# Optimization experiments

Measured on AMD Instinct MI355X. Metric: run time of the kernel, lower is better.

The kernel has to match this reference:

```python
import jax, jax.numpy as jnp
import numpy as np

N_HEADS, N_KV, HEAD_DIM = 16, 4, 64
DIM = 4096
LATENT = N_HEADS * HEAD_DIM   # 1024
KV_DIM = N_KV * HEAD_DIM      # 256
KSZ = 3


def _causal_conv1d(x, w, b, groups):
    # x: [B,S,C]; w: [Cout, Cin//groups, K]; causal left padding (K-1)
    y = jax.lax.conv_general_dilated(
        x.transpose(0, 2, 1), w, window_strides=(1,),
        padding=[(w.shape[-1] - 1, 0)], feature_group_count=groups,
        dimension_numbers=('NCH', 'OIH', 'NCH'))
    return (y + b[None, :, None]).transpose(0, 2, 1)


def _rope(x, cos, sin):
    # x: [B,H,S,D] interleaved pairs; cos/sin: [1,1,S,D//2]
    x1, x2 = x[..., ::2], x[..., 1::2]
    out = jnp.stack([x1 * cos - x2 * sin, x1 * sin + x2 * cos], axis=-1)
    return out.reshape(x.shape)


def _l2norm(x):
    n = jnp.sqrt(jnp.sum(x * x, axis=-1, keepdims=True))
    return x / jnp.maximum(n, 1e-12)


def setup_inputs() -> dict:
    key = jax.random.key(0)
    ks = jax.random.split(key, 12)
    sc = 0.02
    x = jax.random.normal(ks[0], (2, 2048, DIM), jnp.float32)
    w_qkv = jax.random.normal(ks[1], (LATENT + 2 * KV_DIM, DIM), jnp.float32) * sc
    w_o = jax.random.normal(ks[2], (DIM, LATENT), jnp.float32) * sc
    qc1_w = jax.random.normal(ks[3], (LATENT, LATENT // N_HEADS, KSZ), jnp.float32) * sc
    qc1_b = jnp.zeros((LATENT,), jnp.float32)
    qc2_w = jax.random.normal(ks[4], (LATENT, LATENT, KSZ), jnp.float32) * sc
    qc2_b = jnp.zeros((LATENT,), jnp.float32)
    kc1_w = jax.random.normal(ks[5], (KV_DIM, KV_DIM // N_KV, KSZ), jnp.float32) * sc
    kc1_b = jnp.zeros((KV_DIM,), jnp.float32)
    kc2_w = jax.random.normal(ks[6], (KV_DIM, KV_DIM, KSZ), jnp.float32) * sc
    kc2_b = jnp.zeros((KV_DIM,), jnp.float32)
    key_temp = jnp.full((1,), float(HEAD_DIM) ** 0.5, jnp.float32)
    return dict(x=x, w_qkv=w_qkv, w_o=w_o, qc1_w=qc1_w, qc1_b=qc1_b,
                qc2_w=qc2_w, qc2_b=qc2_b, kc1_w=kc1_w, kc1_b=kc1_b,
                kc2_w=kc2_w, kc2_b=kc2_b, key_temp=key_temp)


def _forward(x, w_qkv, w_o, qc1_w, qc1_b, qc2_w, qc2_b, kc1_w, kc1_b, kc2_w, kc2_b, key_temp):
    B, S, _ = x.shape
    qkv = x @ w_qkv.T  # [B,S,LATENT+2*KV_DIM]
    q = qkv[..., :LATENT]
    k = qkv[..., LATENT:LATENT + KV_DIM]
    # value shift: first half current token, second half previous token (0 at t=0)
    half = KV_DIM // 2
    v_curr = qkv[..., LATENT + KV_DIM:LATENT + KV_DIM + half]
    v_prev = qkv[..., LATENT + KV_DIM + half:]
    v = jnp.concatenate([v_curr, jnp.pad(v_prev[:, :-1, :], ((0, 0), (1, 0), (0, 0)))], axis=-1)
    q_pre, k_pre = q, k
    # grouped causal conv sequences on q and k
    q = _causal_conv1d(_causal_conv1d(q, qc1_w, qc1_b, N_HEADS), qc2_w, qc2_b, 1)
    k = _causal_conv1d(_causal_conv1d(k, kc1_w, kc1_b, N_KV), kc2_w, kc2_b, 1)
    # qk-mean coupling (n_groups = 4 branch)
    q_mean = q_pre.reshape(B, S, N_HEADS, HEAD_DIM).mean(axis=2)  # [B,S,hd]
    k_mean = k_pre.reshape(B, S, N_KV, HEAD_DIM).mean(axis=2)
    q = q.reshape(B, S, N_HEADS, HEAD_DIM) + 0.5 * k_mean[:, :, None, :]
    k = k.reshape(B, S, N_KV, HEAD_DIM) + 0.5 * q_mean[:, :, None, :]
    q = q.transpose(0, 2, 1, 3)                                   # [B,H,S,d]
    k = k.transpose(0, 2, 1, 3)                                   # [B,Hkv,S,d]
    v = v.reshape(B, S, N_KV, HEAD_DIM).transpose(0, 2, 1, 3)
    # qk-norm with learned key temperature
    q = _l2norm(q)
    k = _l2norm(k) * key_temp
    # RoPE (interleaved pairs)
    inv = 1.0 / (10000.0 ** (jnp.arange(0, HEAD_DIM, 2, dtype=jnp.float32) / HEAD_DIM))
    ang = jnp.arange(S, dtype=jnp.float32)[:, None] * inv[None, :]  # [S,d/2]
    cos, sin = jnp.cos(ang)[None, None], jnp.sin(ang)[None, None]
    q = _rope(q, cos, sin)
    k = _rope(k, cos, sin)
    # GQA: each kv head repeated n_groups times contiguously
    kg = jnp.repeat(k, N_HEADS // N_KV, axis=1)
    vg = jnp.repeat(v, N_HEADS // N_KV, axis=1)
    scale = HEAD_DIM ** -0.5
    scores = jnp.einsum('bhqd,bhkd->bhqk', q, kg) * scale
    causal = jnp.tril(jnp.ones((S, S), dtype=bool))
    scores = jnp.where(causal[None, None], scores, jnp.finfo(scores.dtype).min)
    attn = jax.nn.softmax(scores, axis=-1)
    out = jnp.einsum('bhqk,bhkd->bhqd', attn, vg)
    out = out.transpose(0, 2, 1, 3).reshape(B, S, LATENT)
    return out @ w_o.T  # output_scale = 1.0


def reference(x, w_qkv, w_o, qc1_w, qc1_b, qc2_w, qc2_b, kc1_w, kc1_b, kc2_w, kc2_b, key_temp):
    return _forward(x, w_qkv, w_o, qc1_w, qc1_b, qc2_w, qc2_b, kc1_w, kc1_b, kc2_w, kc2_b, key_temp)
```

## Files before the change

kernel.cpp:

```cpp
#include <hip/hip_runtime.h>
#include <hip/hip_bf16.h>
#include <cstddef>

#define NB 2
#define SEQ 2048
#define DIMX 4096
#define NH 16
#define NKV 4
#define HD 64
#define LATENT 1024
#define KVD 256
#define QKVN 1536
#define BS (NB*SEQ)
#define SP (SEQ+2)

typedef __attribute__((ext_vector_type(8))) short short8v;
typedef __attribute__((ext_vector_type(4))) float f32x4;
typedef __attribute__((ext_vector_type(4))) unsigned short ushort4v;
typedef __attribute__((ext_vector_type(4))) unsigned int uint4v;

static __device__ __forceinline__ unsigned short f2bf(float f) {
    union { float f; unsigned u; } v; v.f = f;
    unsigned r = v.u + 0x7fffu + ((v.u >> 16) & 1u);
    return (unsigned short)(r >> 16);
}

static __device__ __forceinline__ unsigned cvt_pk_bf16(float lo, float hi) {
    unsigned r;
    asm("v_cvt_pk_bf16_f32 %0, %1, %2" : "=v"(r) : "v"(lo), "v"(hi));
    return r;
}

static __device__ __forceinline__ void gload_lds16(const unsigned short* g, unsigned short* l) {
    __builtin_amdgcn_global_load_lds((const __attribute__((address_space(1))) void*)g,
                                     (__attribute__((address_space(3))) void*)l, 16, 0, 0);
}

#define XC_BLK (BS*DIMX/4/256)
#define WC_BLK (QKVN*DIMX/4/256)
__global__ __launch_bounds__(256)
void cast_inputs(const float* __restrict__ x, unsigned short* __restrict__ xb,
                 const float* __restrict__ wq, unsigned short* __restrict__ wqb)
{
    const int blk = blockIdx.x;
    const float* in; unsigned short* out; int i;
    if (blk < XC_BLK) { in = x; out = xb; i = blk * 256 + threadIdx.x; }
    else              { in = wq; out = wqb; i = (blk - XC_BLK) * 256 + threadIdx.x; }
    const float4 v = *reinterpret_cast<const float4*>(in + (size_t)i * 4);
    ushort4v o = {f2bf(v.x), f2bf(v.y), f2bf(v.z), f2bf(v.w)};
    *reinterpret_cast<ushort4v*>(out + (size_t)i * 4) = o;
}

#define WO_BLK 4096
#define QW_N (LATENT*LATENT*3)
#define QW_BLK 12288
#define KW_N (KVD*KVD*3)
#define KW_BLK 768
#define RT_BLK 256
__global__ __launch_bounds__(256)
void prep_misc(const float* __restrict__ wo, unsigned short* __restrict__ wob,
               const float* __restrict__ qc2w, unsigned short* __restrict__ qc2wr,
               const float* __restrict__ kc2w, unsigned short* __restrict__ kc2wr,
               float2* __restrict__ rtab,
               unsigned short* __restrict__ pq, unsigned short* __restrict__ pk)
{
    const int blk = blockIdx.x, tid = threadIdx.x;
    if (blk < WO_BLK) {
        const int i = blk * 256 + tid;
        const float4 v = *reinterpret_cast<const float4*>(wo + (size_t)i * 4);
        ushort4v o = {f2bf(v.x), f2bf(v.y), f2bf(v.z), f2bf(v.w)};
        *reinterpret_cast<ushort4v*>(wob + (size_t)i * 4) = o;
    } else if (blk < WO_BLK + QW_BLK) {
        const int idx = (blk - WO_BLK) * 256 + tid;
        if (idx < QW_N) {
            const int o = idx / (LATENT * 3), rem = idx % (LATENT * 3);
            const int j = rem / LATENT, c = rem % LATENT;
            qc2wr[idx] = f2bf(qc2w[(size_t)o * LATENT * 3 + c * 3 + j]);
        }
    } else if (blk < WO_BLK + QW_BLK + KW_BLK) {
        const int idx = (blk - WO_BLK - QW_BLK) * 256 + tid;
        if (idx < KW_N) {
            const int o = idx / (KVD * 3), rem = idx % (KVD * 3);
            const int j = rem / KVD, c = rem % KVD;
            kc2wr[idx] = f2bf(kc2w[(size_t)o * KVD * 3 + c * 3 + j]);
        }
    } else if (blk < WO_BLK + QW_BLK + KW_BLK + RT_BLK) {
        const int idx = (blk - WO_BLK - QW_BLK - KW_BLK) * 256 + tid;
        const int s = idx >> 5, i = idx & 31;
        const float inv = powf(10000.f, -(float)(2 * i) * (1.f / HD));
        const float ang = (float)s * inv;
        rtab[idx] = make_float2(cosf(ang), sinf(ang));
    } else {
        const int t = (blk - WO_BLK - QW_BLK - KW_BLK - RT_BLK) * 256 + tid;
        if (t < 2 * 2 * LATENT) {
            const int b = t / (2 * LATENT), r = (t % (2 * LATENT)) / LATENT, c = t % LATENT;
            pq[((size_t)b * SP + r) * LATENT + c] = 0;
        }
        if (t < 2 * 2 * KVD) {
            const int b = t / (2 * KVD), r = (t % (2 * KVD)) / KVD, c = t % KVD;
            pk[((size_t)b * SP + r) * KVD + c] = 0;
        }
    }
}

template<int CONV>
__global__ __launch_bounds__(256)
void gemm_bf16(const unsigned short* __restrict__ A, const unsigned short* __restrict__ W,
               const float* __restrict__ bias, float* __restrict__ C,
               int M, int N, int K, int Cch, int klen, size_t ps1, size_t ps2)
{
    __shared__ unsigned short Abuf[2][128 * 32];
    __shared__ unsigned short Bbuf[2][128 * 32];
    const int gx = gridDim.x;
    const int nwg = gx * gridDim.y;
    const int lin = blockIdx.y * gx + blockIdx.x;
    const int swz = (lin & 7) * (nwg >> 3) + (lin >> 3);
    const int n0 = (swz % gx) * 128, m0 = (swz / gx) * 128;
    const int koff = blockIdx.z * klen;
    C += (blockIdx.z == 1) ? ps1 : (blockIdx.z == 2 ? ps2 : 0);
    const int tid = threadIdx.x;
    const int wave = tid >> 6, lane = tid & 63;
    const int lg = lane >> 4, lr = lane & 15;
    const int wm = (wave & 1) * 64, wn = (wave >> 1) * 64;
    const int sr = wave * 32 + (lane >> 2);
    const int sc = (lane & 3) * 8;
    const int bb = m0 / SEQ, s0 = m0 % SEQ;

    const int NT = klen / 32;
    f32x4 acc[4][4];
    #pragma unroll
    for (int i = 0; i < 4; i++)
        #pragma unroll
        for (int j = 0; j < 4; j++) acc[i][j] = (f32x4){0.f, 0.f, 0.f, 0.f};

    auto stage = [&](int buf, int kt) {
        const int k0 = koff + kt * 32;
        const unsigned short* ga0;
        if (!CONV) {
            ga0 = A + (size_t)(m0 + sr) * K + k0 + sc;
        } else {
            const int j = k0 / Cch, c0 = k0 - j * Cch;
            ga0 = A + (size_t)(bb * SP + s0 + j + sr) * Cch + c0 + sc;
        }
        const unsigned short* gb0 = W + (size_t)(n0 + sr) * K + k0 + sc;
        const size_t astep = (size_t)16 * (CONV ? Cch : K);
        #pragma unroll
        for (int i = 0; i < 2; i++) {
            gload_lds16(ga0 + i * astep, &Abuf[buf][(wave * 2 + i) * 512]);
            gload_lds16(gb0 + (size_t)i * 16 * K, &Bbuf[buf][(wave * 2 + i) * 512]);
        }
    };

    stage(0, 0);
    __syncthreads();
    int cur = 0;
    for (int kt = 0; kt < NT; ++kt) {
        if (kt + 1 < NT) stage(cur ^ 1, kt + 1);
        short8v af[4], bf[4];
        #pragma unroll
        for (int mi = 0; mi < 4; mi++)
            af[mi] = *reinterpret_cast<const short8v*>(&Abuf[cur][(wm + mi * 16 + lr) * 32 + lg * 8]);
        #pragma unroll
        for (int ni = 0; ni < 4; ni++)
            bf[ni] = *reinterpret_cast<const short8v*>(&Bbuf[cur][(wn + ni * 16 + lr) * 32 + lg * 8]);
        #pragma unroll
        for (int mi = 0; mi < 4; mi++)
            #pragma unroll
            for (int ni = 0; ni < 4; ni++)
                acc[mi][ni] = __builtin_amdgcn_mfma_f32_16x16x32_bf16(af[mi], bf[ni], acc[mi][ni], 0, 0, 0);
        __syncthreads();
        cur ^= 1;
    }

    #pragma unroll
    for (int ni = 0; ni < 4; ni++) {
        const int col = n0 + wn + ni * 16 + lr;
        const float bv = bias ? bias[col] : 0.f;
        #pragma unroll
        for (int mi = 0; mi < 4; mi++)
            #pragma unroll
            for (int r = 0; r < 4; r++)
                C[(size_t)(m0 + wm + mi * 16 + lg * 4 + r) * N + col] = acc[mi][ni][r] + bv;
    }
}

__global__ __launch_bounds__(256)
void conv1_grouped(const float* __restrict__ qkv0, const float* __restrict__ qkv1,
                   const float* __restrict__ qw, const float* __restrict__ qb,
                   const float* __restrict__ kw, const float* __restrict__ kb,
                   unsigned short* __restrict__ pq, unsigned short* __restrict__ pk)
{
    const int t0 = blockIdx.x * 64;
    const int b  = blockIdx.y;
    const int z  = blockIdx.z;
    const bool isq = (z < NH);
    const int g  = isq ? z : z - NH;
    const int coloff = isq ? 0 : LATENT;
    const float* w = isq ? qw : kw;
    const float* bias = isq ? qb : kb;
    unsigned short* out = isq ? pq : pk;
    const int CH = isq ? LATENT : KVD;

    __shared__ float xs[66][64];
    for (int idx = threadIdx.x; idx < 66 * 64; idx += 256) {
        const int i = idx >> 6, ic = idx & 63;
        const int tt = t0 + i - 2;
        float v = 0.f;
        if (tt >= 0) {
            const size_t off = (size_t)(b * SEQ + tt) * QKVN + coloff + g * 64 + ic;
            v = qkv0[off] + qkv1[off];
        }
        xs[i][ic] = v;
    }
    __syncthreads();
    const int oc = threadIdx.x & 63;
    const int ibase = (threadIdx.x >> 6) * 16;
    float acc[16];
    const float bv = bias[g * 64 + oc];
    #pragma unroll
    for (int i = 0; i < 16; i++) acc[i] = bv;
    const float* wp = w + (size_t)(g * 64 + oc) * 192;
    for (int ic = 0; ic < 64; ic++) {
        const float w0 = wp[ic * 3 + 0], w1 = wp[ic * 3 + 1], w2 = wp[ic * 3 + 2];
        float xv[18];
        #pragma unroll
        for (int r = 0; r < 18; r++) xv[r] = xs[ibase + r][ic];
        #pragma unroll
        for (int i = 0; i < 16; i++) acc[i] += w0 * xv[i] + w1 * xv[i + 1] + w2 * xv[i + 2];
    }
    #pragma unroll
    for (int i = 0; i < 16; i++)
        out[((size_t)b * SP + 2 + t0 + ibase + i) * CH + g * 64 + oc] = f2bf(acc[i]);
}

__global__ __launch_bounds__(256)
void meanv_vtrans(const float* __restrict__ qkv0, const float* __restrict__ qkv1,
                  float* __restrict__ qmean, float* __restrict__ kmean,
                  unsigned short* __restrict__ vTb)
{
    const int s0 = blockIdx.x * 16;
    const int b  = blockIdx.y;
    const int tid = threadIdx.x;
    const int w = tid >> 6, d = tid & 63;
    __shared__ unsigned short vt[4][16][72];

    #pragma unroll
    for (int i = 0; i < 4; i++) {
        const int s = s0 + w * 4 + i;
        const int t = b * SEQ + s;
        const float* r0 = qkv0 + (size_t)t * QKVN;
        const float* r1 = qkv1 + (size_t)t * QKVN;
        float qs = 0.f;
        #pragma unroll
        for (int h = 0; h < NH; h++) qs += r0[h * 64 + d] + r1[h * 64 + d];
        qmean[(size_t)t * 64 + d] = qs * (1.f / NH);
        float ks = 0.f;
        #pragma unroll
        for (int h = 0; h < NKV; h++) ks += r0[LATENT + h * 64 + d] + r1[LATENT + h * 64 + d];
        kmean[(size_t)t * 64 + d] = ks * (1.f / NKV);
        #pragma unroll
        for (int g = 0; g < 4; g++) {
            float v;
            if (g < 2) {
                v = r0[LATENT + KVD + g * 64 + d] + r1[LATENT + KVD + g * 64 + d];
            } else {
                v = 0.f;
                if (s > 0) {
                    const size_t off = (size_t)(t - 1) * QKVN + LATENT + KVD + 128 + (g - 2) * 64 + d;
                    v = qkv0[off] + qkv1[off];
                }
            }
            vt[g][w * 4 + i][d] = f2bf(v);
        }
    }
    __syncthreads();
    {
        const int g = tid >> 6, dd = tid & 63;
        short8v o0, o1;
        #pragma unroll
        for (int j = 0; j < 8; j++) { o0[j] = (short)vt[g][j][dd]; o1[j] = (short)vt[g][8 + j][dd]; }
        unsigned short* op = vTb + ((size_t)(b * NKV + g) * 64 + dd) * SEQ + s0;
        *reinterpret_cast<short8v*>(op) = o0;
        *reinterpret_cast<short8v*>(op + 8) = o1;
    }
}

__global__ __launch_bounds__(256)
void qk_final(const float* __restrict__ qc2a, const float* __restrict__ qc2b, const float* __restrict__ qc2c,
              const float* __restrict__ kc2a, const float* __restrict__ kc2b,
              const float* __restrict__ qbias, const float* __restrict__ kbias,
              const float* __restrict__ qmean, const float* __restrict__ kmean,
              const float* __restrict__ key_temp, const float2* __restrict__ rtab,
              unsigned short* __restrict__ qTb, unsigned short* __restrict__ kTb)
{
    const int t = blockIdx.x * 4 + (threadIdx.x >> 6);
    const int hh = blockIdx.y;
    const int d = threadIdx.x & 63;
    const int b = t >> 11, s = t & (SEQ - 1);
    float val;
    if (hh < NH) {
        const size_t off = (size_t)t * LATENT + hh * 64 + d;
        val = qc2a[off] + qc2b[off] + qc2c[off] + qbias[hh * 64 + d] + 0.5f * kmean[t * 64 + d];
    } else {
        const size_t off = (size_t)t * KVD + (hh - NH) * 64 + d;
        val = kc2a[off] + kc2b[off] + kbias[(hh - NH) * 64 + d] + 0.5f * qmean[t * 64 + d];
    }
    float ss = val * val;
    #pragma unroll
    for (int off = 32; off >= 1; off >>= 1) ss += __shfl_xor(ss, off);
    const float n = sqrtf(ss);
    val = val / fmaxf(n, 1e-12f);
    if (hh >= NH) val *= key_temp[0];
    const float2 cs = rtab[s * 32 + (d >> 1)];
    const float cv = cs.x, sv = cs.y;
    const float partner = __shfl_xor(val, 1);
    const float x1 = (d & 1) ? partner : val;
    const float x2 = (d & 1) ? val : partner;
    const float o = (d & 1) ? (x1 * sv + x2 * cv) : (x1 * cv - x2 * sv);
    if (hh < NH) qTb[((size_t)(b * NH + hh) * SEQ + s) * 64 + d] = f2bf(o);
    else         kTb[((size_t)(b * NKV + (hh - NH)) * SEQ + s) * 64 + d] = f2bf(o);
}

__global__ __launch_bounds__(256)
void attn_mfma(const unsigned short* __restrict__ qTb, const unsigned short* __restrict__ kTb,
               const unsigned short* __restrict__ vTb,
               unsigned short* __restrict__ pnum, float* __restrict__ pden)
{
    const int wg = blockIdx.x;
    const int qg = wg >> 8;
    const int u = wg & 255;
    const int xcd = u & 7, i = u >> 3;
    const int bh = (xcd << 2) | (i >> 3);
    const int r = i & 7;
    const int p = (qg == 0) ? r : (qg == 1) ? (15 - r) : (qg == 2) ? (16 + r) : (31 - r);
    const int blk = 15 - (p >> 1);
    const int part = p & 1;
    const int half = blk + 1;
    const int cbeg = part * half, cend = cbeg + half;

    const int b = bh >> 4, h = bh & 15, g = h >> 2;
    const int tid = threadIdx.x;
    const int wave = tid >> 6, lane = tid & 63;
    const int lg = lane >> 4, lr = lane & 15;
    const int qt = blk * 4 + wave;
    const int q0 = qt * 32;

    __shared__ __align__(16) unsigned short SB[2][16][512];

    short8v qf[2][2];
    const unsigned short* qbase = qTb + ((size_t)(b * NH + h) * SEQ + q0) * 64;
    #pragma unroll
    for (int mf = 0; mf < 2; mf++)
        #pragma unroll
        for (int dc = 0; dc < 2; dc++)
            qf[mf][dc] = *reinterpret_cast<const short8v*>(qbase + (size_t)(mf * 16 + lr) * 64 + dc * 32 + lg * 8);

    short8v onesf;
    #pragma unroll
    for (int j = 0; j < 8; j++) onesf[j] = (short)0x3F80;

    f32x4 acc[2][4];
    f32x4 accden[2];
    #pragma unroll
    for (int mf = 0; mf < 2; mf++) {
        accden[mf] = (f32x4){0.f, 0.f, 0.f, 0.f};
        #pragma unroll
        for (int dt = 0; dt < 4; dt++) acc[mf][dt] = (f32x4){0.f, 0.f, 0.f, 0.f};
    }

    const unsigned short* kbase = kTb + (size_t)(b * NKV + g) * SEQ * 64;
    const unsigned short* vbase = vTb + (size_t)(b * NKV + g) * 64 * SEQ;
    const float EC = 0.125f * 1.44269504f;
    const int src01 = ((lg & 1) << 5) + lr;
    const int src23 = src01 + 16;
    const bool hi = (lg >= 2);

    auto stage64 = [&](int buf, int cc) {
        const int kb = cc * 64;
        #pragma unroll
        for (int i2 = 0; i2 < 4; i2++) {
            const int ch = wave * 4 + i2;
            const int st = ch >> 3, chl = ch & 7;
            const int k0 = kb + st * 32;
            const unsigned short* src;
            if (chl < 4) src = kbase + (size_t)(k0 + (chl >> 1) * 16 + lr) * 64 + (chl & 1) * 32 + lg * 8;
            else         src = vbase + (size_t)((chl - 4) * 16 + lr) * SEQ + k0 + lg * 8;
            gload_lds16(src, &SB[buf][ch][lane * 8]);
        }
    };

    stage64(0, cbeg);
    __syncthreads();
    int cur = 0;
    for (int cc = cbeg; cc < cend; ++cc) {
        if (cc + 1 < cend) stage64(cur ^ 1, cc + 1);
        #pragma unroll
        for (int st = 0; st < 2; ++st) {
            const int c = cc * 2 + st;
            if (c > qt) continue;
            const int k0 = c * 32;
            short8v kf[2][2], vf[4];
            #pragma unroll
            for (int kt = 0; kt < 2; kt++)
                #pragma unroll
                for (int dc = 0; dc < 2; dc++)
                    kf[kt][dc] = *reinterpret_cast<const short8v*>(&SB[cur][st * 8 + kt * 2 + dc][lane * 8]);
            #pragma unroll
            for (int dt = 0; dt < 4; dt++)
                vf[dt] = *reinterpret_cast<const short8v*>(&SB[cur][st * 8 + 4 + dt][lane * 8]);

            const bool diag = (c == qt);
            #pragma unroll
            for (int mf = 0; mf < 2; mf++) {
                f32x4 z0 = (f32x4){0.f, 0.f, 0.f, 0.f}, z1 = (f32x4){0.f, 0.f, 0.f, 0.f};
                __builtin_amdgcn_s_setprio(1);
                z0 = __builtin_amdgcn_mfma_f32_16x16x32_bf16(kf[0][0], qf[mf][0], z0, 0, 0, 0);
                z0 = __builtin_amdgcn_mfma_f32_16x16x32_bf16(kf[0][1], qf[mf][1], z0, 0, 0, 0);
                z1 = __builtin_amdgcn_mfma_f32_16x16x32_bf16(kf[1][0], qf[mf][0], z1, 0, 0, 0);
                z1 = __builtin_amdgcn_mfma_f32_16x16x32_bf16(kf[1][1], qf[mf][1], z1, 0, 0, 0);
                __builtin_amdgcn_s_setprio(0);
                float p0[4], p1[4];
                #pragma unroll
                for (int rr = 0; rr < 4; rr++) {
                    p0[rr] = exp2f(z0[rr] * EC);
                    p1[rr] = exp2f(z1[rr] * EC);
                }
                if (diag) {
                    const int q = q0 + mf * 16 + lr;
                    #pragma unroll
                    for (int rr = 0; rr < 4; rr++) {
                        if (k0 + 4 * lg + rr > q)      p0[rr] = 0.f;
                        if (k0 + 16 + 4 * lg + rr > q) p1[rr] = 0.f;
                    }
                }
                const unsigned W00 = cvt_pk_bf16(p0[0], p0[1]);
                const unsigned W01 = cvt_pk_bf16(p0[2], p0[3]);
                const unsigned W10 = cvt_pk_bf16(p1[0], p1[1]);
                const unsigned W11 = cvt_pk_bf16(p1[2], p1[3]);
                const unsigned a0 = __shfl(W00, src01), b0 = __shfl(W10, src01);
                const unsigned a1 = __shfl(W01, src01), b1 = __shfl(W11, src01);
                const unsigned a2 = __shfl(W00, src23), b2 = __shfl(W10, src23);
                const unsigned a3 = __shfl(W01, src23), b3 = __shfl(W11, src23);
                uint4v pw;
                pw.x = hi ? b0 : a0;
                pw.y = hi ? b1 : a1;
                pw.z = hi ? b2 : a2;
                pw.w = hi ? b3 : a3;
                const short8v pa = __builtin_bit_cast(short8v, pw);
                __builtin_amdgcn_s_setprio(1);
                #pragma unroll
                for (int dt = 0; dt < 4; dt++)
                    acc[mf][dt] = __builtin_amdgcn_mfma_f32_16x16x32_bf16(pa, vf[dt], acc[mf][dt], 0, 0, 0);
                accden[mf] = __builtin_amdgcn_mfma_f32_16x16x32_bf16(pa, onesf, accden[mf], 0, 0, 0);
                __builtin_amdgcn_s_setprio(0);
            }
        }
        __syncthreads();
        cur ^= 1;
    }

    const int base = ((bh * 64 + qt) * 2 + part);
    if (lr == 0) {
        #pragma unroll
        for (int mf = 0; mf < 2; mf++)
            #pragma unroll
            for (int rr = 0; rr < 4; rr++)
                pden[base * 32 + mf * 16 + 4 * lg + rr] = accden[mf][rr];
    }
    unsigned short* np = pnum + (size_t)base * 2048;
    #pragma unroll
    for (int mf = 0; mf < 2; mf++)
        #pragma unroll
        for (int dt = 0; dt < 4; dt++)
            #pragma unroll
            for (int rr = 0; rr < 4; rr++)
                np[(mf * 16 + 4 * lg + rr) * 64 + dt * 16 + lr] = f2bf(acc[mf][dt][rr]);
}

__global__ __launch_bounds__(256)
void attn_merge(const unsigned short* __restrict__ pnum, const float* __restrict__ pden,
                unsigned short* __restrict__ attnb)
{
    const int idx = blockIdx.x * 256 + threadIdx.x;
    const int d0 = (idx & 7) * 8;
    const int qr = (idx >> 3) & 31;
    const int qt = (idx >> 8) & 63;
    const int bh = idx >> 14;
    const int base = (bh * 64 + qt) * 2;
    const float den = pden[base * 32 + qr] + pden[(base + 1) * 32 + qr];
    const float inv = 1.f / den;
    const short8v n0 = *reinterpret_cast<const short8v*>(pnum + (size_t)base * 2048 + qr * 64 + d0);
    const short8v n1 = *reinterpret_cast<const short8v*>(pnum + (size_t)(base + 1) * 2048 + qr * 64 + d0);
    short8v ov;
    #pragma unroll
    for (int j = 0; j < 8; j++) {
        union { unsigned u; float f; } t0, t1;
        t0.u = ((unsigned)(unsigned short)n0[j]) << 16;
        t1.u = ((unsigned)(unsigned short)n1[j]) << 16;
        ov[j] = (short)f2bf((t0.f + t1.f) * inv);
    }
    const int q = qt * 32 + qr;
    const int b = bh >> 4, h = bh & 15;
    *reinterpret_cast<short8v*>(attnb + (size_t)(b * SEQ + q) * LATENT + h * 64 + d0) = ov;
}

extern "C" void kernel_launch(void* const* d_in, const int* in_sizes, int n_in,
                              void* d_out, int out_size, void* d_ws, size_t ws_size,
                              hipStream_t stream)
{
    const float* x       = (const float*)d_in[0];
    const float* w_qkv   = (const float*)d_in[1];
    const float* w_o     = (const float*)d_in[2];
    const float* qc1_w   = (const float*)d_in[3];
    const float* qc1_b   = (const float*)d_in[4];
    const float* qc2_w   = (const float*)d_in[5];
    const float* qc2_b   = (const float*)d_in[6];
    const float* kc1_w   = (const float*)d_in[7];
    const float* kc1_b   = (const float*)d_in[8];
    const float* kc2_w   = (const float*)d_in[9];
    const float* kc2_b   = (const float*)d_in[10];
    const float* key_temp = (const float*)d_in[11];

    char* wsb = (char*)d_ws;
    float* qkv = (float*)wsb;                 wsb += (size_t)BS * QKVN * 4;
    float* qc2 = qkv;
    float* kc2 = (float*)((char*)qkv + (size_t)BS * LATENT * 4);
    unsigned short* pq  = (unsigned short*)wsb;  wsb += (size_t)NB * SP * LATENT * 2;
    unsigned short* pk  = (unsigned short*)wsb;  wsb += (size_t)NB * SP * KVD * 2;
    float* qmean = (float*)wsb;  wsb += (size_t)BS * HD * 4;
    float* kmean = (float*)wsb;  wsb += (size_t)BS * HD * 4;
    unsigned short* qTb  = (unsigned short*)wsb;  wsb += (size_t)BS * LATENT * 2;
    unsigned short* kTb  = (unsigned short*)wsb;  wsb += (size_t)BS * KVD * 2;
    unsigned short* vRow = (unsigned short*)wsb;  wsb += (size_t)BS * KVD * 2;
    unsigned short* vTb  = (unsigned short*)wsb;  wsb += (size_t)BS * KVD * 2;
    unsigned short* xb   = (unsigned short*)wsb;  wsb += (size_t)BS * DIMX * 2;
    unsigned short* attnb  = xb;
    unsigned short* qc2wr  = (unsigned short*)((char*)xb + (size_t)BS * LATENT * 2);
    unsigned short* kc2wr  = (unsigned short*)((char*)qc2wr + (size_t)LATENT * LATENT * 3 * 2);
    unsigned short* wqkvb = (unsigned short*)wsb;  wsb += (size_t)QKVN * DIMX * 2;
    unsigned short* wob   = wqkvb;
    (void)vRow;

    float* outp = (float*)d_out;

    float* qkvp1 = outp;
    const size_t QKV_PS = (size_t)((ptrdiff_t)(qkvp1 - qkv));
    float* qc2p1 = (float*)((char*)d_ws + 67512320);
    float* qc2p2 = outp;
    const size_t QC2_PS1 = (size_t)(qc2p1 - qc2);
    const size_t QC2_PS2 = (size_t)((ptrdiff_t)(qc2p2 - qc2));
    float* kc2p1 = (float*)((char*)d_ws + (size_t)BS * QKVN * 4);
    const size_t KC2_PS1 = (size_t)(kc2p1 - kc2);
    float2* rtab = (float2*)((char*)d_ws + 84289536);
    unsigned short* apnum = (unsigned short*)d_ws;
    float* apden = (float*)((char*)d_ws + 16777216);

    cast_inputs<<<dim3(XC_BLK + WC_BLK), 256, 0, stream>>>(x, xb, w_qkv, wqkvb);
    gemm_bf16<0><<<dim3(QKVN / 128, BS / 128, 2), 256, 0, stream>>>(xb, wqkvb, nullptr, qkv, BS, QKVN, DIMX, 0, DIMX / 2, QKV_PS, 0);
    prep_misc<<<dim3(WO_BLK + QW_BLK + KW_BLK + RT_BLK + 16), 256, 0, stream>>>(
        w_o, wob, qc2_w, qc2wr, kc2_w, kc2wr, rtab, pq, pk);
    meanv_vtrans<<<dim3(SEQ / 16, NB), 256, 0, stream>>>(qkv, qkvp1, qmean, kmean, vTb);
    conv1_grouped<<<dim3(SEQ / 64, NB, NH + NKV), 256, 0, stream>>>(qkv, qkvp1, qc1_w, qc1_b, kc1_w, kc1_b, pq, pk);
    gemm_bf16<1><<<dim3(LATENT / 128, BS / 128, 3), 256, 0, stream>>>(pq, qc2wr, nullptr, qc2, BS, LATENT, LATENT * 3, LATENT, LATENT, QC2_PS1, QC2_PS2);
    gemm_bf16<1><<<dim3(KVD / 128, BS / 128, 2), 256, 0, stream>>>(pk, kc2wr, nullptr, kc2, BS, KVD, KVD * 3, KVD, KVD * 3 / 2, KC2_PS1, 0);
    qk_final<<<dim3(BS / 4, NH + NKV), 256, 0, stream>>>(qc2, qc2p1, qc2p2, kc2, kc2p1, qc2_b, kc2_b,
                                                         qmean, kmean, key_temp, rtab, qTb, kTb);
    attn_mfma<<<dim3(1024), 256, 0, stream>>>(qTb, kTb, vTb, apnum, apden);
    attn_merge<<<dim3(2048), 256, 0, stream>>>(apnum, apden, attnb);
    gemm_bf16<0><<<dim3(DIMX / 128, BS / 128, 1), 256, 0, stream>>>(attnb, wob, nullptr, outp, BS, DIMX, LATENT, 0, LATENT, 0, 0);
}
```

Before: 339.0 us.

## Split attention KV range into four parts per query block

The attention kernel now splits each query block's causal KV range into four partitions instead of two and launches twice as many workgroups, ordering them longest-first. The merge kernel sums four partial numerators and denominators. The intent is better load balance and occupancy across CUs on the attention stage. The cost is extra partial-result traffic, a heavier merge, and some empty partitions for short rows.

```diff
diff --git a/kernel.cpp b/kernel.cpp
--- a/kernel.cpp
+++ b/kernel.cpp
@@ -327,16 +327,16 @@
                unsigned short* __restrict__ pnum, float* __restrict__ pden)
 {
     const int wg = blockIdx.x;
-    const int qg = wg >> 8;
+    const int o = wg >> 8;
     const int u = wg & 255;
     const int xcd = u & 7, i = u >> 3;
     const int bh = (xcd << 2) | (i >> 3);
-    const int r = i & 7;
-    const int p = (qg == 0) ? r : (qg == 1) ? (15 - r) : (qg == 2) ? (16 + r) : (31 - r);
-    const int blk = 15 - (p >> 1);
-    const int part = p & 1;
-    const int half = blk + 1;
-    const int cbeg = part * half, cend = cbeg + half;
+    const int rr0 = i & 7;
+    const int v = (o < 4) ? (63 - ((o << 3) + rr0)) : (((o - 4) << 3) + rr0);
+    const int blk = v >> 2;
+    const int part = v & 3;
+    const int T = 2 * (blk + 1);
+    const int cbeg = (part * T) >> 2, cend = ((part + 1) * T) >> 2;
 
     const int b = bh >> 4, h = bh & 15, g = h >> 2;
     const int tid = threadIdx.x;
@@ -389,77 +389,79 @@
         }
     };
 
-    stage64(0, cbeg);
-    __syncthreads();
-    int cur = 0;
-    for (int cc = cbeg; cc < cend; ++cc) {
-        if (cc + 1 < cend) stage64(cur ^ 1, cc + 1);
-        #pragma unroll
-        for (int st = 0; st < 2; ++st) {
-            const int c = cc * 2 + st;
-            if (c > qt) continue;
-            const int k0 = c * 32;
-            short8v kf[2][2], vf[4];
+    if (cbeg < cend) {
+        stage64(0, cbeg);
+        __syncthreads();
+        int cur = 0;
+        for (int cc = cbeg; cc < cend; ++cc) {
+            if (cc + 1 < cend) stage64(cur ^ 1, cc + 1);
             #pragma unroll
-            for (int kt = 0; kt < 2; kt++)
+            for (int st = 0; st < 2; ++st) {
+                const int c = cc * 2 + st;
+                if (c > qt) continue;
+                const int k0 = c * 32;
+                short8v kf[2][2], vf[4];
                 #pragma unroll
-                for (int dc = 0; dc < 2; dc++)
-                    kf[kt][dc] = *reinterpret_cast<const short8v*>(&SB[cur][st * 8 + kt * 2 + dc][lane * 8]);
-            #pragma unroll
-            for (int dt = 0; dt < 4; dt++)
-                vf[dt] = *reinterpret_cast<const short8v*>(&SB[cur][st * 8 + 4 + dt][lane * 8]);
-
-            const bool diag = (c == qt);
-            #pragma unroll
-            for (int mf = 0; mf < 2; mf++) {
-                f32x4 z0 = (f32x4){0.f, 0.f, 0.f, 0.f}, z1 = (f32x4){0.f, 0.f, 0.f, 0.f};
-                __builtin_amdgcn_s_setprio(1);
-                z0 = __builtin_amdgcn_mfma_f32_16x16x32_bf16(kf[0][0], qf[mf][0], z0, 0, 0, 0);
-                z0 = __builtin_amdgcn_mfma_f32_16x16x32_bf16(kf[0][1], qf[mf][1], z0, 0, 0, 0);
-                z1 = __builtin_amdgcn_mfma_f32_16x16x32_bf16(kf[1][0], qf[mf][0], z1, 0, 0, 0);
-                z1 = __builtin_amdgcn_mfma_f32_16x16x32_bf16(kf[1][1], qf[mf][1], z1, 0, 0, 0);
-                __builtin_amdgcn_s_setprio(0);
-                float p0[4], p1[4];
+                for (int kt = 0; kt < 2; kt++)
+                    #pragma unroll
+                    for (int dc = 0; dc < 2; dc++)
+                        kf[kt][dc] = *reinterpret_cast<const short8v*>(&SB[cur][st * 8 + kt * 2 + dc][lane * 8]);
                 #pragma unroll
-                for (int rr = 0; rr < 4; rr++) {
-                    p0[rr] = exp2f(z0[rr] * EC);
-                    p1[rr] = exp2f(z1[rr] * EC);
-                }
-                if (diag) {
-                    const int q = q0 + mf * 16 + lr;
+                for (int dt = 0; dt < 4; dt++)
+                    vf[dt] = *reinterpret_cast<const short8v*>(&SB[cur][st * 8 + 4 + dt][lane * 8]);
+
+                const bool diag = (c == qt);
+                #pragma unroll
+                for (int mf = 0; mf < 2; mf++) {
+                    f32x4 z0 = (f32x4){0.f, 0.f, 0.f, 0.f}, z1 = (f32x4){0.f, 0.f, 0.f, 0.f};
+                    __builtin_amdgcn_s_setprio(1);
+                    z0 = __builtin_amdgcn_mfma_f32_16x16x32_bf16(kf[0][0], qf[mf][0], z0, 0, 0, 0);
+                    z0 = __builtin_amdgcn_mfma_f32_16x16x32_bf16(kf[0][1], qf[mf][1], z0, 0, 0, 0);
+                    z1 = __builtin_amdgcn_mfma_f32_16x16x32_bf16(kf[1][0], qf[mf][0], z1, 0, 0, 0);
+                    z1 = __builtin_amdgcn_mfma_f32_16x16x32_bf16(kf[1][1], qf[mf][1], z1, 0, 0, 0);
+                    __builtin_amdgcn_s_setprio(0);
+                    float p0[4], p1[4];
                     #pragma unroll
                     for (int rr = 0; rr < 4; rr++) {
-                        if (k0 + 4 * lg + rr > q)      p0[rr] = 0.f;
-                        if (k0 + 16 + 4 * lg + rr > q) p1[rr] = 0.f;
+                        p0[rr] = exp2f(z0[rr] * EC);
+                        p1[rr] = exp2f(z1[rr] * EC);
                     }
+                    if (diag) {
+                        const int q = q0 + mf * 16 + lr;
+                        #pragma unroll
+                        for (int rr = 0; rr < 4; rr++) {
+                            if (k0 + 4 * lg + rr > q)      p0[rr] = 0.f;
+                            if (k0 + 16 + 4 * lg + rr > q) p1[rr] = 0.f;
+                        }
+                    }
+                    const unsigned W00 = cvt_pk_bf16(p0[0], p0[1]);
+                    const unsigned W01 = cvt_pk_bf16(p0[2], p0[3]);
+                    const unsigned W10 = cvt_pk_bf16(p1[0], p1[1]);
+                    const unsigned W11 = cvt_pk_bf16(p1[2], p1[3]);
+                    const unsigned a0 = __shfl(W00, src01), b0 = __shfl(W10, src01);
+                    const unsigned a1 = __shfl(W01, src01), b1 = __shfl(W11, src01);
+                    const unsigned a2 = __shfl(W00, src23), b2 = __shfl(W10, src23);
+                    const unsigned a3 = __shfl(W01, src23), b3 = __shfl(W11, src23);
+                    uint4v pw;
+                    pw.x = hi ? b0 : a0;
+                    pw.y = hi ? b1 : a1;
+                    pw.z = hi ? b2 : a2;
+                    pw.w = hi ? b3 : a3;
+                    const short8v pa = __builtin_bit_cast(short8v, pw);
+                    __builtin_amdgcn_s_setprio(1);
+                    #pragma unroll
+                    for (int dt = 0; dt < 4; dt++)
+                        acc[mf][dt] = __builtin_amdgcn_mfma_f32_16x16x32_bf16(pa, vf[dt], acc[mf][dt], 0, 0, 0);
+                    accden[mf] = __builtin_amdgcn_mfma_f32_16x16x32_bf16(pa, onesf, accden[mf], 0, 0, 0);
+                    __builtin_amdgcn_s_setprio(0);
                 }
-                const unsigned W00 = cvt_pk_bf16(p0[0], p0[1]);
-                const unsigned W01 = cvt_pk_bf16(p0[2], p0[3]);
-                const unsigned W10 = cvt_pk_bf16(p1[0], p1[1]);
-                const unsigned W11 = cvt_pk_bf16(p1[2], p1[3]);
-                const unsigned a0 = __shfl(W00, src01), b0 = __shfl(W10, src01);
-                const unsigned a1 = __shfl(W01, src01), b1 = __shfl(W11, src01);
-                const unsigned a2 = __shfl(W00, src23), b2 = __shfl(W10, src23);
-                const unsigned a3 = __shfl(W01, src23), b3 = __shfl(W11, src23);
-                uint4v pw;
-                pw.x = hi ? b0 : a0;
-                pw.y = hi ? b1 : a1;
-                pw.z = hi ? b2 : a2;
-                pw.w = hi ? b3 : a3;
-                const short8v pa = __builtin_bit_cast(short8v, pw);
-                __builtin_amdgcn_s_setprio(1);
-                #pragma unroll
-                for (int dt = 0; dt < 4; dt++)
-                    acc[mf][dt] = __builtin_amdgcn_mfma_f32_16x16x32_bf16(pa, vf[dt], acc[mf][dt], 0, 0, 0);
-                accden[mf] = __builtin_amdgcn_mfma_f32_16x16x32_bf16(pa, onesf, accden[mf], 0, 0, 0);
-                __builtin_amdgcn_s_setprio(0);
             }
-        }
-        __syncthreads();
-        cur ^= 1;
-    }
-
-    const int base = ((bh * 64 + qt) * 2 + part);
+            __syncthreads();
+            cur ^= 1;
+        }
+    }
+
+    const int base = ((bh * 64 + qt) * 4 + part);
     if (lr == 0) {
         #pragma unroll
         for (int mf = 0; mf < 2; mf++)
@@ -486,19 +488,24 @@
     const int qr = (idx >> 3) & 31;
     const int qt = (idx >> 8) & 63;
     const int bh = idx >> 14;
-    const int base = (bh * 64 + qt) * 2;
-    const float den = pden[base * 32 + qr] + pden[(base + 1) * 32 + qr];
+    const int base = (bh * 64 + qt) * 4;
+    float den = 0.f;
+    float s[8] = {0.f, 0.f, 0.f, 0.f, 0.f, 0.f, 0.f, 0.f};
+    #pragma unroll
+    for (int p = 0; p < 4; p++) {
+        den += pden[(base + p) * 32 + qr];
+        const short8v nv = *reinterpret_cast<const short8v*>(pnum + (size_t)(base + p) * 2048 + qr * 64 + d0);
+        #pragma unroll
+        for (int j = 0; j < 8; j++) {
+            union { unsigned u; float f; } tt;
+            tt.u = ((unsigned)(unsigned short)nv[j]) << 16;
+            s[j] += tt.f;
+        }
+    }
     const float inv = 1.f / den;
-    const short8v n0 = *reinterpret_cast<const short8v*>(pnum + (size_t)base * 2048 + qr * 64 + d0);
-    const short8v n1 = *reinterpret_cast<const short8v*>(pnum + (size_t)(base + 1) * 2048 + qr * 64 + d0);
     short8v ov;
     #pragma unroll
-    for (int j = 0; j < 8; j++) {
-        union { unsigned u; float f; } t0, t1;
-        t0.u = ((unsigned)(unsigned short)n0[j]) << 16;
-        t1.u = ((unsigned)(unsigned short)n1[j]) << 16;
-        ov[j] = (short)f2bf((t0.f + t1.f) * inv);
-    }
+    for (int j = 0; j < 8; j++) ov[j] = (short)f2bf(s[j] * inv);
     const int q = qt * 32 + qr;
     const int b = bh >> 4, h = bh & 15;
     *reinterpret_cast<short8v*>(attnb + (size_t)(b * SEQ + q) * LATENT + h * 64 + d0) = ov;
@@ -553,7 +560,7 @@
     const size_t KC2_PS1 = (size_t)(kc2p1 - kc2);
     float2* rtab = (float2*)((char*)d_ws + 84289536);
     unsigned short* apnum = (unsigned short*)d_ws;
-    float* apden = (float*)((char*)d_ws + 16777216);
+    float* apden = (float*)((char*)d_ws + 33562624);
 
     cast_inputs<<<dim3(XC_BLK + WC_BLK), 256, 0, stream>>>(x, xb, w_qkv, wqkvb);
     gemm_bf16<0><<<dim3(QKVN / 128, BS / 128, 2), 256, 0, stream>>>(xb, wqkvb, nullptr, qkv, BS, QKVN, DIMX, 0, DIMX / 2, QKV_PS, 0);
@@ -565,7 +572,7 @@
     gemm_bf16<1><<<dim3(KVD / 128, BS / 128, 2), 256, 0, stream>>>(pk, kc2wr, nullptr, kc2, BS, KVD, KVD * 3, KVD, KVD * 3 / 2, KC2_PS1, 0);
     qk_final<<<dim3(BS / 4, NH + NKV), 256, 0, stream>>>(qc2, qc2p1, qc2p2, kc2, kc2p1, qc2_b, kc2_b,
                                                          qmean, kmean, key_temp, rtab, qTb, kTb);
-    attn_mfma<<<dim3(1024), 256, 0, stream>>>(qTb, kTb, vTb, apnum, apden);
+    attn_mfma<<<dim3(2048), 256, 0, stream>>>(qTb, kTb, vTb, apnum, apden);
     attn_merge<<<dim3(2048), 256, 0, stream>>>(apnum, apden, attnb);
     gemm_bf16<0><<<dim3(DIMX / 128, BS / 128, 1), 256, 0, stream>>>(attnb, wob, nullptr, outp, BS, DIMX, LATENT, 0, LATENT, 0, 0);
 }
```

New measurement: 345.2 us. About the same (+1.8%).
